# Kernel tuning notes

Measured on AMD Instinct MI355X. Metric: run time of the kernel, lower is better.

The kernel has to match this reference:

```python
import jax, jax.numpy as jnp
import numpy as np

E_LOCAL = 8          # num_experts // ep_size
HIDDEN = 2048
INTER = 1408
M_TOTAL = 8192       # routed tokens on this rank (balanced: 1024 per expert)
BLOCK_N = 128
BLOCK_K = 128


def _dequant_blocked(w, s, bn=BLOCK_N, bk=BLOCK_K):
    """Per-[bn,bk]-block dequant: w[e,n,k] * s[e, n//bn, k//bk].
    Equivalent to the in-accumulator blockwise scaling in the triton kernel,
    since the scale is constant within each (n-block, k-block) tile."""
    E, N, K = w.shape
    wb = w.reshape(E, N // bn, bn, K // bk, bk)
    return (wb * s[:, :, None, :, None]).reshape(E, N, K)


def setup_inputs() -> dict:
    key = jax.random.key(0)
    k1, k2, k3, k4, k5 = jax.random.split(key, 5)
    hidden_states = jax.random.normal(k1, (M_TOTAL, HIDDEN), dtype=jnp.float32)
    # balanced dispatch: equal token count per local expert (tokens sorted by expert)
    tokens_per_expert = jnp.full((E_LOCAL,), M_TOTAL // E_LOCAL, dtype=jnp.int32)
    # fp8 quantized weight values (simulated as f32) + per-128x128-block scales
    gate_up_weight = jax.random.normal(k2, (E_LOCAL, 2 * INTER, HIDDEN), dtype=jnp.float32)
    gate_up_scale = jax.random.uniform(k3, (E_LOCAL, 2 * INTER // BLOCK_N, HIDDEN // BLOCK_K),
                                       dtype=jnp.float32, minval=0.01, maxval=0.05)
    gate_down_weight = jax.random.normal(k4, (E_LOCAL, HIDDEN, INTER), dtype=jnp.float32)
    gate_down_scale = jax.random.uniform(k5, (E_LOCAL, HIDDEN // BLOCK_N, INTER // BLOCK_K),
                                         dtype=jnp.float32, minval=0.01, maxval=0.05)
    return {
        "hidden_states": hidden_states,
        "tokens_per_expert": tokens_per_expert,
        "gate_up_weight": gate_up_weight,
        "gate_up_scale": gate_up_scale,
        "gate_down_weight": gate_down_weight,
        "gate_down_scale": gate_down_scale,
    }


def reference(hidden_states, tokens_per_expert, gate_up_weight, gate_up_scale,
              gate_down_weight, gate_down_scale):
    E, N1, K = gate_up_weight.shape   # N1 = 2*intermediate
    M = hidden_states.shape[0]
    m_per_e = M // E                  # balanced segments (tokens sorted by expert)
    inter = N1 // 2

    # NOTE on per-token activation quant: the original quantizes `a` per
    # (token, 128-wide k-group) with scale = amax/fp8_max and the kernel
    # multiplies the same scale back in the accumulator; in real arithmetic
    # quant->dequant cancels, so we feed hidden_states directly.

    # ---- grouped GEMM 1 (gate_up), blocked fp8 dequant fused as pre-scale ----
    w1 = _dequant_blocked(gate_up_weight, gate_up_scale)         # [E, 2I, K]
    a = hidden_states.reshape(E, m_per_e, K)                     # segment view
    gateup = jnp.einsum('emk,enk->emn', a, w1)                   # [E, m, 2I]

    # ---- silu_and_mul ----
    gate, up = gateup[..., :inter], gateup[..., inter:]
    down_in = jax.nn.silu(gate) * up                             # [E, m, I]

    # ---- grouped GEMM 2 (down), blocked fp8 dequant ----
    w2 = _dequant_blocked(gate_down_weight, gate_down_scale)     # [E, H, I]
    out = jnp.einsum('emi,ehi->emh', down_in, w2)                # [E, m, H]
    return out.reshape(M, -1)
```

## Files before the change

kernel.cpp:

```cpp
#include <hip/hip_runtime.h>
#include <hip/hip_bf16.h>
#include <cstdint>

#define E_LOCAL 8
#define HIDDEN  2048
#define INTER   1408
#define MPE     1024
#define BK      64
#define LDP     72

typedef __attribute__((ext_vector_type(8))) __bf16 bf16x8;
typedef __attribute__((ext_vector_type(4))) float  f32x4;
typedef __attribute__((ext_vector_type(8))) unsigned short u16x8;

__device__ __forceinline__ unsigned short f2b(float f) {
    unsigned int u = __float_as_uint(f);
    unsigned int r = (u + 0x7fffu + ((u >> 16) & 1u)) >> 16;
    return (unsigned short)r;
}

__device__ __forceinline__ void async16(const unsigned short* g, unsigned short* l) {
    __builtin_amdgcn_global_load_lds(
        (const __attribute__((address_space(1))) unsigned int*)g,
        (__attribute__((address_space(3))) unsigned int*)l, 16, 0, 0);
}

__global__ __launch_bounds__(256) void convert_kernel(
        const float* __restrict__ src, const float* __restrict__ scale,
        unsigned short* __restrict__ dst, int N, int K, int K16, int NB, int KBl)
{
    const int e = blockIdx.y;
    unsigned int idx = blockIdx.x * 256u + threadIdx.x;
    unsigned int r   = idx / (unsigned int)K16;
    unsigned int c16 = idx - r * (unsigned int)K16;
    size_t base = ((size_t)e * N + r) * K + (size_t)c16 * 16;
    float4 v0 = *(const float4*)(src + base);
    float4 v1 = *(const float4*)(src + base + 4);
    float4 v2 = *(const float4*)(src + base + 8);
    float4 v3 = *(const float4*)(src + base + 12);
    float s = 1.0f;
    if (scale) s = scale[((size_t)e * NB + (r >> 7)) * KBl + (c16 >> 3)];
    u16x8 o0, o1;
    o0[0] = f2b(v0.x * s); o0[1] = f2b(v0.y * s); o0[2] = f2b(v0.z * s); o0[3] = f2b(v0.w * s);
    o0[4] = f2b(v1.x * s); o0[5] = f2b(v1.y * s); o0[6] = f2b(v1.z * s); o0[7] = f2b(v1.w * s);
    o1[0] = f2b(v2.x * s); o1[1] = f2b(v2.y * s); o1[2] = f2b(v2.z * s); o1[3] = f2b(v2.w * s);
    o1[4] = f2b(v3.x * s); o1[5] = f2b(v3.y * s); o1[6] = f2b(v3.z * s); o1[7] = f2b(v3.w * s);
    *(u16x8*)(dst + base)     = o0;
    *(u16x8*)(dst + base + 8) = o1;
}

__global__ __launch_bounds__(256, 2) void gemm1_bf16(
        const unsigned short* __restrict__ bh,
        const unsigned short* __restrict__ bw1,
        unsigned short* __restrict__ down_in)
{
    __shared__ alignas(16) unsigned short sA[128 * 64];
    __shared__ alignas(16) unsigned short sG[128 * 64];
    __shared__ alignas(16) unsigned short sU[128 * 64];

    const int my = blockIdx.x;
    const int nx = blockIdx.y;
    const int e  = blockIdx.z;
    const int t  = threadIdx.x;
    const int lane = t & 63;
    const int wave = t >> 6;
    const int wm   = (wave >> 1) * 64;
    const int wn   = (wave & 1) * 64;
    const int l16  = lane & 15;
    const int quad = lane >> 4;
    const int xq   = l16 & 7;

    const unsigned short* Abase = bh  + ((size_t)e * MPE + (size_t)my * 128) * HIDDEN;
    const unsigned short* Gbase = bw1 + ((size_t)e * (2 * INTER) + (size_t)nx * 128) * HIDDEN;
    const unsigned short* Ubase = Gbase + (size_t)INTER * HIDDEN;

    const int lr  = lane >> 3;
    const int c8g = (lane & 7) ^ (lr & 7);
    const size_t lgoff = (size_t)(wave * 32 + lr) * HIDDEN + (size_t)c8g * 8;
    const int ldsbase = wave * 2048;

    f32x4 accg[4][4], accu[4][4];
    #pragma unroll
    for (int i = 0; i < 4; ++i)
        #pragma unroll
        for (int j = 0; j < 4; ++j) { accg[i][j] = {0,0,0,0}; accu[i][j] = {0,0,0,0}; }

    for (int kt = 0; kt < HIDDEN / BK; ++kt) {
        const int k0 = kt * BK;
        __syncthreads();
        #pragma unroll
        for (int j = 0; j < 4; ++j) {
            const size_t go = lgoff + (size_t)j * 8 * HIDDEN + k0;
            const int lo = ldsbase + j * 512;
            async16(Abase + go, &sA[lo]);
            async16(Gbase + go, &sG[lo]);
            async16(Ubase + go, &sU[lo]);
        }
        __syncthreads();

        #pragma unroll
        for (int kk = 0; kk < 2; ++kk) {
            bf16x8 af[4], gf[4], uf[4];
            const int cb = ((kk * 4 + quad) ^ xq) * 8;
            #pragma unroll
            for (int i = 0; i < 4; ++i) {
                af[i] = *(const bf16x8*)&sA[(wm + i * 16 + l16) * 64 + cb];
                gf[i] = *(const bf16x8*)&sG[(wn + i * 16 + l16) * 64 + cb];
                uf[i] = *(const bf16x8*)&sU[(wn + i * 16 + l16) * 64 + cb];
            }
            #pragma unroll
            for (int mi = 0; mi < 4; ++mi)
                #pragma unroll
                for (int ni = 0; ni < 4; ++ni) {
                    accg[mi][ni] = __builtin_amdgcn_mfma_f32_16x16x32_bf16(af[mi], gf[ni], accg[mi][ni], 0, 0, 0);
                    accu[mi][ni] = __builtin_amdgcn_mfma_f32_16x16x32_bf16(af[mi], uf[ni], accu[mi][ni], 0, 0, 0);
                }
        }
    }

    unsigned short* Obase = down_in + ((size_t)e * MPE + (size_t)my * 128) * INTER + (size_t)nx * 128;
    #pragma unroll
    for (int mi = 0; mi < 4; ++mi)
        #pragma unroll
        for (int ni = 0; ni < 4; ++ni)
            #pragma unroll
            for (int r = 0; r < 4; ++r) {
                float g = accg[mi][ni][r];
                float u = accu[mi][ni][r];
                float d = g / (1.f + __expf(-g)) * u;
                int m = wm + mi * 16 + quad * 4 + r;
                int c = wn + ni * 16 + l16;
                Obase[(size_t)m * INTER + c] = f2b(d);
            }
}

__global__ __launch_bounds__(256, 2) void gemm2_bf16(
        const unsigned short* __restrict__ down_in,
        const unsigned short* __restrict__ bw2,
        float* __restrict__ out)
{
    __shared__ alignas(16) unsigned short sA[128 * 64];
    __shared__ alignas(16) unsigned short sW[128 * 64];

    const int my = blockIdx.x;
    const int nx = blockIdx.y;
    const int e  = blockIdx.z;
    const int t  = threadIdx.x;
    const int lane = t & 63;
    const int wave = t >> 6;
    const int wm   = (wave >> 1) * 64;
    const int wn   = (wave & 1) * 64;
    const int l16  = lane & 15;
    const int quad = lane >> 4;
    const int xq   = l16 & 7;

    const unsigned short* Abase = down_in + ((size_t)e * MPE + (size_t)my * 128) * INTER;
    const unsigned short* Wbase = bw2 + ((size_t)e * HIDDEN + (size_t)nx * 128) * INTER;

    const int lr  = lane >> 3;
    const int c8g = (lane & 7) ^ (lr & 7);
    const size_t lgoff = (size_t)(wave * 32 + lr) * INTER + (size_t)c8g * 8;
    const int ldsbase = wave * 2048;

    f32x4 acc[4][4];
    #pragma unroll
    for (int i = 0; i < 4; ++i)
        #pragma unroll
        for (int j = 0; j < 4; ++j) acc[i][j] = {0,0,0,0};

    for (int kt = 0; kt < INTER / BK; ++kt) {
        const int k0 = kt * BK;
        __syncthreads();
        #pragma unroll
        for (int j = 0; j < 4; ++j) {
            const size_t go = lgoff + (size_t)j * 8 * INTER + k0;
            const int lo = ldsbase + j * 512;
            async16(Abase + go, &sA[lo]);
            async16(Wbase + go, &sW[lo]);
        }
        __syncthreads();

        #pragma unroll
        for (int kk = 0; kk < 2; ++kk) {
            bf16x8 af[4], wf[4];
            const int cb = ((kk * 4 + quad) ^ xq) * 8;
            #pragma unroll
            for (int i = 0; i < 4; ++i) {
                af[i] = *(const bf16x8*)&sA[(wm + i * 16 + l16) * 64 + cb];
                wf[i] = *(const bf16x8*)&sW[(wn + i * 16 + l16) * 64 + cb];
            }
            #pragma unroll
            for (int mi = 0; mi < 4; ++mi)
                #pragma unroll
                for (int ni = 0; ni < 4; ++ni)
                    acc[mi][ni] = __builtin_amdgcn_mfma_f32_16x16x32_bf16(af[mi], wf[ni], acc[mi][ni], 0, 0, 0);
        }
    }

    float* Obase = out + ((size_t)e * MPE + (size_t)my * 128) * HIDDEN + (size_t)nx * 128;
    #pragma unroll
    for (int mi = 0; mi < 4; ++mi)
        #pragma unroll
        for (int ni = 0; ni < 4; ++ni)
            #pragma unroll
            for (int r = 0; r < 4; ++r) {
                int m = wm + mi * 16 + quad * 4 + r;
                int c = wn + ni * 16 + l16;
                Obase[(size_t)m * HIDDEN + c] = acc[mi][ni][r];
            }
}

__global__ __launch_bounds__(256, 2) void gemm1_f32(
        const float* __restrict__ hidden, const float* __restrict__ w1,
        const float* __restrict__ s1, unsigned short* __restrict__ down_in)
{
    __shared__ unsigned short sA[128 * LDP];
    __shared__ unsigned short sG[128 * LDP];
    __shared__ unsigned short sU[128 * LDP];
    const int nx = blockIdx.x, my = blockIdx.y, e = blockIdx.z;
    const int t = threadIdx.x, lane = t & 63, wave = t >> 6;
    const int wm = (wave >> 1) * 64, wn = (wave & 1) * 64;
    const int l16 = lane & 15, quad = lane >> 4;
    const float* Abase = hidden + ((size_t)e * MPE + (size_t)my * 128) * HIDDEN;
    const float* Gbase = w1 + ((size_t)e * (2 * INTER) + (size_t)nx * 128) * HIDDEN;
    const float* Ubase = w1 + ((size_t)e * (2 * INTER) + INTER + (size_t)nx * 128) * HIDDEN;
    f32x4 accg[4][4], accu[4][4];
    #pragma unroll
    for (int i = 0; i < 4; ++i)
        #pragma unroll
        for (int j = 0; j < 4; ++j) { accg[i][j] = {0,0,0,0}; accu[i][j] = {0,0,0,0}; }
    for (int kt = 0; kt < HIDDEN / BK; ++kt) {
        const int k0 = kt * BK;
        const int kb = k0 >> 7;
        const float sg = s1[(e * 22 + nx) * 16 + kb];
        const float su = s1[(e * 22 + 11 + nx) * 16 + kb];
        __syncthreads();
        #pragma unroll
        for (int i = 0; i < 8; ++i) {
            int idx = i * 256 + t; int r = idx >> 4, c4 = idx & 15;
            float4 v = *(const float4*)(Abase + (size_t)r * HIDDEN + k0 + c4 * 4);
            ushort4 p = { f2b(v.x), f2b(v.y), f2b(v.z), f2b(v.w) };
            *(ushort4*)&sA[r * LDP + c4 * 4] = p;
        }
        #pragma unroll
        for (int i = 0; i < 8; ++i) {
            int idx = i * 256 + t; int r = idx >> 4, c4 = idx & 15;
            float4 v = *(const float4*)(Gbase + (size_t)r * HIDDEN + k0 + c4 * 4);
            ushort4 p = { f2b(v.x * sg), f2b(v.y * sg), f2b(v.z * sg), f2b(v.w * sg) };
            *(ushort4*)&sG[r * LDP + c4 * 4] = p;
        }
        #pragma unroll
        for (int i = 0; i < 8; ++i) {
            int idx = i * 256 + t; int r = idx >> 4, c4 = idx & 15;
            float4 v = *(const float4*)(Ubase + (size_t)r * HIDDEN + k0 + c4 * 4);
            ushort4 p = { f2b(v.x * su), f2b(v.y * su), f2b(v.z * su), f2b(v.w * su) };
            *(ushort4*)&sU[r * LDP + c4 * 4] = p;
        }
        __syncthreads();
        #pragma unroll
        for (int kk = 0; kk < BK; kk += 32) {
            bf16x8 af[4], gf[4], uf[4];
            #pragma unroll
            for (int i = 0; i < 4; ++i) {
                af[i] = *(const bf16x8*)&sA[(wm + i * 16 + l16) * LDP + kk + quad * 8];
                gf[i] = *(const bf16x8*)&sG[(wn + i * 16 + l16) * LDP + kk + quad * 8];
                uf[i] = *(const bf16x8*)&sU[(wn + i * 16 + l16) * LDP + kk + quad * 8];
            }
            #pragma unroll
            for (int mi = 0; mi < 4; ++mi)
                #pragma unroll
                for (int ni = 0; ni < 4; ++ni) {
                    accg[mi][ni] = __builtin_amdgcn_mfma_f32_16x16x32_bf16(af[mi], gf[ni], accg[mi][ni], 0, 0, 0);
                    accu[mi][ni] = __builtin_amdgcn_mfma_f32_16x16x32_bf16(af[mi], uf[ni], accu[mi][ni], 0, 0, 0);
                }
        }
    }
    unsigned short* Obase = down_in + ((size_t)e * MPE + (size_t)my * 128) * INTER + (size_t)nx * 128;
    #pragma unroll
    for (int mi = 0; mi < 4; ++mi)
        #pragma unroll
        for (int ni = 0; ni < 4; ++ni)
            #pragma unroll
            for (int r = 0; r < 4; ++r) {
                float g = accg[mi][ni][r], u = accu[mi][ni][r];
                float d = g / (1.f + __expf(-g)) * u;
                int m = wm + mi * 16 + quad * 4 + r, c = wn + ni * 16 + l16;
                Obase[(size_t)m * INTER + c] = f2b(d);
            }
}

__global__ __launch_bounds__(256, 2) void gemm2_f32(
        const unsigned short* __restrict__ down_in, const float* __restrict__ w2,
        const float* __restrict__ s2, float* __restrict__ out)
{
    __shared__ unsigned short sA[128 * LDP];
    __shared__ unsigned short sW[128 * LDP];
    const int nx = blockIdx.x, my = blockIdx.y, e = blockIdx.z;
    const int t = threadIdx.x, lane = t & 63, wave = t >> 6;
    const int wm = (wave >> 1) * 64, wn = (wave & 1) * 64;
    const int l16 = lane & 15, quad = lane >> 4;
    const unsigned short* Abase = down_in + ((size_t)e * MPE + (size_t)my * 128) * INTER;
    const float* Wbase = w2 + ((size_t)e * HIDDEN + (size_t)nx * 128) * INTER;
    f32x4 acc[4][4];
    #pragma unroll
    for (int i = 0; i < 4; ++i)
        #pragma unroll
        for (int j = 0; j < 4; ++j) acc[i][j] = {0,0,0,0};
    for (int kt = 0; kt < INTER / BK; ++kt) {
        const int k0 = kt * BK;
        const float sc = s2[(e * 16 + nx) * 11 + (k0 >> 7)];
        __syncthreads();
        #pragma unroll
        for (int i = 0; i < 4; ++i) {
            int idx = i * 256 + t; int r = idx >> 3, c8 = idx & 7;
            uint4 v = *(const uint4*)(Abase + (size_t)r * INTER + k0 + c8 * 8);
            *(uint4*)&sA[r * LDP + c8 * 8] = v;
        }
        #pragma unroll
        for (int i = 0; i < 8; ++i) {
            int idx = i * 256 + t; int r = idx >> 4, c4 = idx & 15;
            float4 v = *(const float4*)(Wbase + (size_t)r * INTER + k0 + c4 * 4);
            ushort4 p = { f2b(v.x * sc), f2b(v.y * sc), f2b(v.z * sc), f2b(v.w * sc) };
            *(ushort4*)&sW[r * LDP + c4 * 4] = p;
        }
        __syncthreads();
        #pragma unroll
        for (int kk = 0; kk < BK; kk += 32) {
            bf16x8 af[4], wf[4];
            #pragma unroll
            for (int i = 0; i < 4; ++i) {
                af[i] = *(const bf16x8*)&sA[(wm + i * 16 + l16) * LDP + kk + quad * 8];
                wf[i] = *(const bf16x8*)&sW[(wn + i * 16 + l16) * LDP + kk + quad * 8];
            }
            #pragma unroll
            for (int mi = 0; mi < 4; ++mi)
                #pragma unroll
                for (int ni = 0; ni < 4; ++ni)
                    acc[mi][ni] = __builtin_amdgcn_mfma_f32_16x16x32_bf16(af[mi], wf[ni], acc[mi][ni], 0, 0, 0);
        }
    }
    float* Obase = out + ((size_t)e * MPE + (size_t)my * 128) * HIDDEN + (size_t)nx * 128;
    #pragma unroll
    for (int mi = 0; mi < 4; ++mi)
        #pragma unroll
        for (int ni = 0; ni < 4; ++ni)
            #pragma unroll
            for (int r = 0; r < 4; ++r) {
                int m = wm + mi * 16 + quad * 4 + r, c = wn + ni * 16 + l16;
                Obase[(size_t)m * HIDDEN + c] = acc[mi][ni][r];
            }
}

extern "C" void kernel_launch(void* const* d_in, const int* in_sizes, int n_in,
                              void* d_out, int out_size, void* d_ws, size_t ws_size,
                              hipStream_t stream) {
    const float* hidden = (const float*)d_in[0];
    const float* w1 = (const float*)d_in[2];
    const float* s1 = (const float*)d_in[3];
    const float* w2 = (const float*)d_in[4];
    const float* s2 = (const float*)d_in[5];
    float* out = (float*)d_out;

    const size_t SZ_BH  = (size_t)8192 * HIDDEN * 2;
    const size_t SZ_BW1 = (size_t)E_LOCAL * 2 * INTER * HIDDEN * 2;
    const size_t SZ_BW2 = (size_t)E_LOCAL * HIDDEN * INTER * 2;
    const size_t SZ_DI  = (size_t)E_LOCAL * MPE * INTER * 2;
    const size_t NEED = SZ_BH + SZ_BW1 + SZ_BW2 + SZ_DI;

    dim3 blk(256);
    if (ws_size >= NEED) {
        char* w = (char*)d_ws;
        unsigned short* bh      = (unsigned short*)w;            w += SZ_BH;
        unsigned short* bw1     = (unsigned short*)w;            w += SZ_BW1;
        unsigned short* bw2     = (unsigned short*)w;            w += SZ_BW2;
        unsigned short* down_in = (unsigned short*)w;

        convert_kernel<<<dim3(4096, 1), blk, 0, stream>>>(hidden, nullptr, bh, 8192, HIDDEN, HIDDEN / 16, 0, 0);
        convert_kernel<<<dim3(1408, E_LOCAL), blk, 0, stream>>>(w1, s1, bw1, 2 * INTER, HIDDEN, HIDDEN / 16, 22, 16);
        convert_kernel<<<dim3(704, E_LOCAL), blk, 0, stream>>>(w2, s2, bw2, HIDDEN, INTER, INTER / 16, 16, 11);

        gemm1_bf16<<<dim3(MPE / 128, INTER / 128, E_LOCAL), blk, 0, stream>>>(bh, bw1, down_in);
        gemm2_bf16<<<dim3(MPE / 128, HIDDEN / 128, E_LOCAL), blk, 0, stream>>>(down_in, bw2, out);
    } else {
        unsigned short* down_in = (unsigned short*)d_ws;
        gemm1_f32<<<dim3(INTER / 128, MPE / 128, E_LOCAL), blk, 0, stream>>>(hidden, w1, s1, down_in);
        gemm2_f32<<<dim3(HIDDEN / 128, MPE / 128, E_LOCAL), blk, 0, stream>>>(down_in, w2, s2, out);
    }
}
```

Before: 586.2 us.

## Double-buffer GEMM K-loop with BK=32, merge conversion kernels into one launch

Both bf16 GEMM kernels now use a two-stage LDS ping-pong with a K tile of 32. The next tile's async global-to-LDS loads are issued before the MFMAs on the current tile, which removes one barrier per iteration and overlaps memory with compute. MFMA sections are wrapped in s_setprio, and the three weight/activation conversion launches are fused into a single flat launch. The smaller K tile means more iterations and barriers, and the new XOR swizzle changes the LDS bank access pattern.

```diff
diff --git a/kernel.cpp b/kernel.cpp
--- a/kernel.cpp
+++ b/kernel.cpp
@@ -25,21 +25,43 @@
         (__attribute__((address_space(3))) unsigned int*)l, 16, 0, 0);
 }
 
-__global__ __launch_bounds__(256) void convert_kernel(
-        const float* __restrict__ src, const float* __restrict__ scale,
-        unsigned short* __restrict__ dst, int N, int K, int K16, int NB, int KBl)
+#define CONV_C0 1048576u
+#define CONV_C1 2883584u
+#define CONV_C2 1441792u
+#define CONV_BLOCKS ((CONV_C0 + CONV_C1 + CONV_C2) / 256u)
+
+__global__ __launch_bounds__(256) void convert_all(
+        const float* __restrict__ hidden, const float* __restrict__ w1,
+        const float* __restrict__ s1, const float* __restrict__ w2,
+        const float* __restrict__ s2,
+        unsigned short* __restrict__ bh, unsigned short* __restrict__ bw1,
+        unsigned short* __restrict__ bw2)
 {
-    const int e = blockIdx.y;
-    unsigned int idx = blockIdx.x * 256u + threadIdx.x;
-    unsigned int r   = idx / (unsigned int)K16;
-    unsigned int c16 = idx - r * (unsigned int)K16;
-    size_t base = ((size_t)e * N + r) * K + (size_t)c16 * 16;
+    unsigned int g = blockIdx.x * 256u + threadIdx.x;
+    const float* src; unsigned short* dst; size_t base; float s;
+    if (g < CONV_C0) {
+        unsigned int r = g >> 7, c16 = g & 127u;
+        base = ((size_t)r << 11) + (size_t)c16 * 16;
+        s = 1.0f; src = hidden; dst = bh;
+    } else if (g < CONV_C0 + CONV_C1) {
+        unsigned int li = g - CONV_C0;
+        unsigned int r = li >> 7, c16 = li & 127u;
+        unsigned int e = r / 2816u, n = r - e * 2816u;
+        base = ((size_t)r << 11) + (size_t)c16 * 16;
+        s = s1[(e * 22u + (n >> 7)) * 16u + (c16 >> 3)];
+        src = w1; dst = bw1;
+    } else {
+        unsigned int li = g - CONV_C0 - CONV_C1;
+        unsigned int r = li / 88u, c16 = li - r * 88u;
+        unsigned int e = r >> 11, h = r & 2047u;
+        base = (size_t)r * 1408 + (size_t)c16 * 16;
+        s = s2[(e * 16u + (h >> 7)) * 11u + (c16 >> 3)];
+        src = w2; dst = bw2;
+    }
     float4 v0 = *(const float4*)(src + base);
     float4 v1 = *(const float4*)(src + base + 4);
     float4 v2 = *(const float4*)(src + base + 8);
     float4 v3 = *(const float4*)(src + base + 12);
-    float s = 1.0f;
-    if (scale) s = scale[((size_t)e * NB + (r >> 7)) * KBl + (c16 >> 3)];
     u16x8 o0, o1;
     o0[0] = f2b(v0.x * s); o0[1] = f2b(v0.y * s); o0[2] = f2b(v0.z * s); o0[3] = f2b(v0.w * s);
     o0[4] = f2b(v1.x * s); o0[5] = f2b(v1.y * s); o0[6] = f2b(v1.z * s); o0[7] = f2b(v1.w * s);
@@ -54,9 +76,9 @@
         const unsigned short* __restrict__ bw1,
         unsigned short* __restrict__ down_in)
 {
-    __shared__ alignas(16) unsigned short sA[128 * 64];
-    __shared__ alignas(16) unsigned short sG[128 * 64];
-    __shared__ alignas(16) unsigned short sU[128 * 64];
+    __shared__ alignas(16) unsigned short sA[2][128 * 32];
+    __shared__ alignas(16) unsigned short sG[2][128 * 32];
+    __shared__ alignas(16) unsigned short sU[2][128 * 32];
 
     const int my = blockIdx.x;
     const int nx = blockIdx.y;
@@ -68,16 +90,16 @@
     const int wn   = (wave & 1) * 64;
     const int l16  = lane & 15;
     const int quad = lane >> 4;
-    const int xq   = l16 & 7;
 
     const unsigned short* Abase = bh  + ((size_t)e * MPE + (size_t)my * 128) * HIDDEN;
     const unsigned short* Gbase = bw1 + ((size_t)e * (2 * INTER) + (size_t)nx * 128) * HIDDEN;
     const unsigned short* Ubase = Gbase + (size_t)INTER * HIDDEN;
 
-    const int lr  = lane >> 3;
-    const int c8g = (lane & 7) ^ (lr & 7);
-    const size_t lgoff = (size_t)(wave * 32 + lr) * HIDDEN + (size_t)c8g * 8;
-    const int ldsbase = wave * 2048;
+    const int cgo = (((lane & 3) ^ ((lane >> 3) & 3)) * 8);
+    const size_t g0 = (size_t)(wave * 32 + (lane >> 2)) * HIDDEN + cgo;
+    const int lo0 = wave * 1024 + lane * 8;
+
+    const int cb = ((quad ^ ((l16 >> 1) & 3)) * 8);
 
     f32x4 accg[4][4], accu[4][4];
     #pragma unroll
@@ -85,37 +107,38 @@
         #pragma unroll
         for (int j = 0; j < 4; ++j) { accg[i][j] = {0,0,0,0}; accu[i][j] = {0,0,0,0}; }
 
-    for (int kt = 0; kt < HIDDEN / BK; ++kt) {
-        const int k0 = kt * BK;
-        __syncthreads();
-        #pragma unroll
-        for (int j = 0; j < 4; ++j) {
-            const size_t go = lgoff + (size_t)j * 8 * HIDDEN + k0;
-            const int lo = ldsbase + j * 512;
-            async16(Abase + go, &sA[lo]);
-            async16(Gbase + go, &sG[lo]);
-            async16(Ubase + go, &sU[lo]);
-        }
-        __syncthreads();
-
-        #pragma unroll
-        for (int kk = 0; kk < 2; ++kk) {
-            bf16x8 af[4], gf[4], uf[4];
-            const int cb = ((kk * 4 + quad) ^ xq) * 8;
-            #pragma unroll
-            for (int i = 0; i < 4; ++i) {
-                af[i] = *(const bf16x8*)&sA[(wm + i * 16 + l16) * 64 + cb];
-                gf[i] = *(const bf16x8*)&sG[(wn + i * 16 + l16) * 64 + cb];
-                uf[i] = *(const bf16x8*)&sU[(wn + i * 16 + l16) * 64 + cb];
-            }
-            #pragma unroll
-            for (int mi = 0; mi < 4; ++mi)
-                #pragma unroll
-                for (int ni = 0; ni < 4; ++ni) {
-                    accg[mi][ni] = __builtin_amdgcn_mfma_f32_16x16x32_bf16(af[mi], gf[ni], accg[mi][ni], 0, 0, 0);
-                    accu[mi][ni] = __builtin_amdgcn_mfma_f32_16x16x32_bf16(af[mi], uf[ni], accu[mi][ni], 0, 0, 0);
-                }
-        }
+    auto stage = [&](int buf, int kt) {
+        const size_t go = g0 + (size_t)kt * 32;
+        async16(Abase + go,               &sA[buf][lo0]);
+        async16(Abase + go + 16 * HIDDEN, &sA[buf][lo0 + 512]);
+        async16(Gbase + go,               &sG[buf][lo0]);
+        async16(Gbase + go + 16 * HIDDEN, &sG[buf][lo0 + 512]);
+        async16(Ubase + go,               &sU[buf][lo0]);
+        async16(Ubase + go + 16 * HIDDEN, &sU[buf][lo0 + 512]);
+    };
+
+    stage(0, 0);
+    #pragma unroll 2
+    for (int kt = 0; kt < HIDDEN / 32; ++kt) {
+        const int cur = kt & 1;
+        __syncthreads();
+        if (kt + 1 < HIDDEN / 32) stage(cur ^ 1, kt + 1);
+        bf16x8 af[4], gf[4], uf[4];
+        #pragma unroll
+        for (int i = 0; i < 4; ++i) {
+            af[i] = *(const bf16x8*)&sA[cur][(wm + i * 16 + l16) * 32 + cb];
+            gf[i] = *(const bf16x8*)&sG[cur][(wn + i * 16 + l16) * 32 + cb];
+            uf[i] = *(const bf16x8*)&sU[cur][(wn + i * 16 + l16) * 32 + cb];
+        }
+        __builtin_amdgcn_s_setprio(1);
+        #pragma unroll
+        for (int mi = 0; mi < 4; ++mi)
+            #pragma unroll
+            for (int ni = 0; ni < 4; ++ni) {
+                accg[mi][ni] = __builtin_amdgcn_mfma_f32_16x16x32_bf16(af[mi], gf[ni], accg[mi][ni], 0, 0, 0);
+                accu[mi][ni] = __builtin_amdgcn_mfma_f32_16x16x32_bf16(af[mi], uf[ni], accu[mi][ni], 0, 0, 0);
+            }
+        __builtin_amdgcn_s_setprio(0);
     }
 
     unsigned short* Obase = down_in + ((size_t)e * MPE + (size_t)my * 128) * INTER + (size_t)nx * 128;
@@ -139,8 +162,8 @@
         const unsigned short* __restrict__ bw2,
         float* __restrict__ out)
 {
-    __shared__ alignas(16) unsigned short sA[128 * 64];
-    __shared__ alignas(16) unsigned short sW[128 * 64];
+    __shared__ alignas(16) unsigned short sA[2][128 * 32];
+    __shared__ alignas(16) unsigned short sW[2][128 * 32];
 
     const int my = blockIdx.x;
     const int nx = blockIdx.y;
@@ -152,15 +175,14 @@
     const int wn   = (wave & 1) * 64;
     const int l16  = lane & 15;
     const int quad = lane >> 4;
-    const int xq   = l16 & 7;
 
     const unsigned short* Abase = down_in + ((size_t)e * MPE + (size_t)my * 128) * INTER;
     const unsigned short* Wbase = bw2 + ((size_t)e * HIDDEN + (size_t)nx * 128) * INTER;
 
-    const int lr  = lane >> 3;
-    const int c8g = (lane & 7) ^ (lr & 7);
-    const size_t lgoff = (size_t)(wave * 32 + lr) * INTER + (size_t)c8g * 8;
-    const int ldsbase = wave * 2048;
+    const int cgo = (((lane & 3) ^ ((lane >> 3) & 3)) * 8);
+    const size_t g0 = (size_t)(wave * 32 + (lane >> 2)) * INTER + cgo;
+    const int lo0 = wave * 1024 + lane * 8;
+    const int cb  = ((quad ^ ((l16 >> 1) & 3)) * 8);
 
     f32x4 acc[4][4];
     #pragma unroll
@@ -168,33 +190,33 @@
         #pragma unroll
         for (int j = 0; j < 4; ++j) acc[i][j] = {0,0,0,0};
 
-    for (int kt = 0; kt < INTER / BK; ++kt) {
-        const int k0 = kt * BK;
-        __syncthreads();
-        #pragma unroll
-        for (int j = 0; j < 4; ++j) {
-            const size_t go = lgoff + (size_t)j * 8 * INTER + k0;
-            const int lo = ldsbase + j * 512;
-            async16(Abase + go, &sA[lo]);
-            async16(Wbase + go, &sW[lo]);
-        }
-        __syncthreads();
-
-        #pragma unroll
-        for (int kk = 0; kk < 2; ++kk) {
-            bf16x8 af[4], wf[4];
-            const int cb = ((kk * 4 + quad) ^ xq) * 8;
-            #pragma unroll
-            for (int i = 0; i < 4; ++i) {
-                af[i] = *(const bf16x8*)&sA[(wm + i * 16 + l16) * 64 + cb];
-                wf[i] = *(const bf16x8*)&sW[(wn + i * 16 + l16) * 64 + cb];
-            }
-            #pragma unroll
-            for (int mi = 0; mi < 4; ++mi)
-                #pragma unroll
-                for (int ni = 0; ni < 4; ++ni)
-                    acc[mi][ni] = __builtin_amdgcn_mfma_f32_16x16x32_bf16(af[mi], wf[ni], acc[mi][ni], 0, 0, 0);
-        }
+    auto stage = [&](int buf, int kt) {
+        const size_t go = g0 + (size_t)kt * 32;
+        async16(Abase + go,              &sA[buf][lo0]);
+        async16(Abase + go + 16 * INTER, &sA[buf][lo0 + 512]);
+        async16(Wbase + go,              &sW[buf][lo0]);
+        async16(Wbase + go + 16 * INTER, &sW[buf][lo0 + 512]);
+    };
+
+    stage(0, 0);
+    #pragma unroll 2
+    for (int kt = 0; kt < INTER / 32; ++kt) {
+        const int cur = kt & 1;
+        __syncthreads();
+        if (kt + 1 < INTER / 32) stage(cur ^ 1, kt + 1);
+        bf16x8 af[4], wf[4];
+        #pragma unroll
+        for (int i = 0; i < 4; ++i) {
+            af[i] = *(const bf16x8*)&sA[cur][(wm + i * 16 + l16) * 32 + cb];
+            wf[i] = *(const bf16x8*)&sW[cur][(wn + i * 16 + l16) * 32 + cb];
+        }
+        __builtin_amdgcn_s_setprio(1);
+        #pragma unroll
+        for (int mi = 0; mi < 4; ++mi)
+            #pragma unroll
+            for (int ni = 0; ni < 4; ++ni)
+                acc[mi][ni] = __builtin_amdgcn_mfma_f32_16x16x32_bf16(af[mi], wf[ni], acc[mi][ni], 0, 0, 0);
+        __builtin_amdgcn_s_setprio(0);
     }
 
     float* Obase = out + ((size_t)e * MPE + (size_t)my * 128) * HIDDEN + (size_t)nx * 128;
@@ -375,9 +397,7 @@
         unsigned short* bw2     = (unsigned short*)w;            w += SZ_BW2;
         unsigned short* down_in = (unsigned short*)w;
 
-        convert_kernel<<<dim3(4096, 1), blk, 0, stream>>>(hidden, nullptr, bh, 8192, HIDDEN, HIDDEN / 16, 0, 0);
-        convert_kernel<<<dim3(1408, E_LOCAL), blk, 0, stream>>>(w1, s1, bw1, 2 * INTER, HIDDEN, HIDDEN / 16, 22, 16);
-        convert_kernel<<<dim3(704, E_LOCAL), blk, 0, stream>>>(w2, s2, bw2, HIDDEN, INTER, INTER / 16, 16, 11);
+        convert_all<<<dim3(CONV_BLOCKS), blk, 0, stream>>>(hidden, w1, s1, w2, s2, bh, bw1, bw2);
 
         gemm1_bf16<<<dim3(MPE / 128, INTER / 128, E_LOCAL), blk, 0, stream>>>(bh, bw1, down_in);
         gemm2_bf16<<<dim3(MPE / 128, HIDDEN / 128, E_LOCAL), blk, 0, stream>>>(down_in, bw2, out);
```

Result: slower. 605.3 us (+3.3%).
